# Optimization experiments

Hardware: AMD Instinct MI355X
Metric: run time of the kernel (lower is better)

The kernel has to match this reference:

```python
import jax, jax.numpy as jnp
import numpy as np

L, H, D, M = 2, 8, 64, 64   # layers, heads, query dim, value dim
DM = H * M                  # d_model = 512
FF = 1024                   # feed-forward dim
B, S, F_IN = 8, 4096, 586   # batch, seq_len, input feature dim
EPS_ATTN = 1e-6             # fast_transformers LinearAttention eps
EPS_LN = 1e-5               # torch LayerNorm default eps


def setup_inputs() -> dict:
    key = jax.random.key(0)
    ks = jax.random.split(key, 16)
    p = lambda k, shape: jax.random.normal(k, shape, jnp.float32) * 0.02
    return {
        "embeddings": jax.random.normal(ks[0], (B, S, F_IN), jnp.float32),
        "W0": p(ks[1], (F_IN, DM)), "b0": jnp.zeros((DM,), jnp.float32),
        "Wq": p(ks[2], (L, DM, DM)), "bq": jnp.zeros((L, DM), jnp.float32),
        "Wk": p(ks[3], (L, DM, DM)), "bk": jnp.zeros((L, DM), jnp.float32),
        "Wv": p(ks[4], (L, DM, DM)), "bv": jnp.zeros((L, DM), jnp.float32),
        "Wo": p(ks[5], (L, DM, DM)), "bo": jnp.zeros((L, DM), jnp.float32),
        "ln1_s": jnp.ones((L, DM), jnp.float32), "ln1_b": jnp.zeros((L, DM), jnp.float32),
        "W1": p(ks[6], (L, DM, FF)), "b1": jnp.zeros((L, FF), jnp.float32),
        "W2": p(ks[7], (L, FF, DM)), "b2": jnp.zeros((L, DM), jnp.float32),
        "ln2_s": jnp.ones((L, DM), jnp.float32), "ln2_b": jnp.zeros((L, DM), jnp.float32),
        "lnf_s": jnp.ones((DM,), jnp.float32), "lnf_b": jnp.zeros((DM,), jnp.float32),
        "Wout": p(ks[8], (DM, 1)), "bout": jnp.zeros((1,), jnp.float32),
    }


def _ln(x, s, b):
    mu = x.mean(-1, keepdims=True)
    var = ((x - mu) ** 2).mean(-1, keepdims=True)
    return (x - mu) * jax.lax.rsqrt(var + EPS_LN) * s + b


def _feat(x):
    # elu feature map of fast_transformers linear attention
    return jax.nn.elu(x) + 1.0


def reference(embeddings, W0, b0, Wq, bq, Wk, bk, Wv, bv, Wo, bo,
              ln1_s, ln1_b, W1, b1, W2, b2, ln2_s, ln2_b,
              lnf_s, lnf_b, Wout, bout):
    x = embeddings @ W0 + b0                       # [B,S,DM]
    Bn, Sn = x.shape[0], x.shape[1]
    for l in range(L):
        q = _feat((x @ Wq[l] + bq[l]).reshape(Bn, Sn, H, D))
        k = _feat((x @ Wk[l] + bk[l]).reshape(Bn, Sn, H, D))
        v = (x @ Wv[l] + bv[l]).reshape(Bn, Sn, H, M)
        # non-causal linear attention: O(S) in sequence length
        kv = jnp.einsum("bshd,bshm->bhdm", k, v)                    # [B,H,D,M]
        z = 1.0 / (jnp.einsum("blhd,bhd->blh", q, k.sum(1)) + EPS_ATTN)
        a = jnp.einsum("blhd,bhdm,blh->blhm", q, kv, z).reshape(Bn, Sn, DM)
        x = x + a @ Wo[l] + bo[l]                  # residual (dropout=0 eval)
        x = _ln(x, ln1_s[l], ln1_b[l])
        y = jax.nn.relu(x @ W1[l] + b1[l]) @ W2[l] + b2[l]
        x = _ln(x + y, ln2_s[l], ln2_b[l])
    x = _ln(x, lnf_s, lnf_b)                        # final encoder LayerNorm
    return (x @ Wout + bout)[..., 0]                # squeeze -> [B,S]
```

## Files before the change

### kernel.cpp

```cpp
#include <hip/hip_runtime.h>
#include <hip/hip_bf16.h>
#include <math.h>

typedef unsigned short u16;
typedef short s16x8 __attribute__((ext_vector_type(8)));
typedef float f32x4 __attribute__((ext_vector_type(4)));

#define BS_   32768
#define SEQ_  4096
#define DM_   512
#define FF_   1024
#define FIN_  586
#define FINP_ 608
#define PADC  136
#define PADB  520
#define NCH   8

__device__ __forceinline__ u16 f2b(float f) {
    __hip_bfloat16 h = __float2bfloat16(f);
    return *reinterpret_cast<u16*>(&h);
}
__device__ __forceinline__ float b2f(u16 h) {
    union { unsigned u; float f; } a; a.u = ((unsigned)h) << 16;
    return a.f;
}

typedef __attribute__((address_space(1))) const unsigned gu32;
typedef __attribute__((address_space(3))) unsigned lu32;
__device__ __forceinline__ void glds16(const void* g, void* l) {
    __builtin_amdgcn_global_load_lds((gu32*)g, (lu32*)l, 16, 0, 0);
}

__device__ __forceinline__ void tr_tile(const float* __restrict__ W, u16* __restrict__ Wt,
                                        int K, int N, int Kpad, int tidx, int ktiles,
                                        float (*t)[33]) {
    int kb = (tidx % ktiles) << 5, nb = (tidx / ktiles) << 5;
    int tx = threadIdx.x, ty = threadIdx.y;
#pragma unroll
    for (int j = 0; j < 32; j += 8) {
        int k = kb + ty + j;
        t[ty + j][tx] = (k < K) ? W[(size_t)k * N + nb + tx] : 0.f;
    }
    __syncthreads();
#pragma unroll
    for (int j = 0; j < 32; j += 8) {
        Wt[(size_t)(nb + ty + j) * Kpad + kb + tx] = f2b(t[tx][ty + j]);
    }
}

__global__ void k_tr_all(const float* __restrict__ W0, const float* __restrict__ Wq,
                         const float* __restrict__ Wk, const float* __restrict__ Wv,
                         const float* __restrict__ Wo, const float* __restrict__ W1,
                         const float* __restrict__ W2,
                         u16* __restrict__ W0t, u16* __restrict__ Wqkv,
                         u16* __restrict__ Wot, u16* __restrict__ W1t,
                         u16* __restrict__ W2t) {
    __shared__ float t[32][33];
    int b = blockIdx.x;
    if (b < 304) { tr_tile(W0, W0t, FIN_, DM_, FINP_, b, 19, t); return; }
    b -= 304;
    int l = b >> 11;
    int r = b & 2047;
    if (r < 768) {
        int sel = r >> 8, ti = r & 255;
        const float* src = sel == 0 ? Wq : (sel == 1 ? Wk : Wv);
        tr_tile(src + (size_t)l * 262144, Wqkv + (size_t)l * 786432 + (size_t)sel * 262144,
                512, 512, 512, ti, 16, t);
    } else if (r < 1024) {
        tr_tile(Wo + (size_t)l * 262144, Wot + (size_t)l * 262144, 512, 512, 512, r - 768, 16, t);
    } else if (r < 1536) {
        tr_tile(W1 + (size_t)l * 524288, W1t + (size_t)l * 524288, 512, 1024, 512, r - 1024, 16, t);
    } else {
        tr_tile(W2 + (size_t)l * 524288, W2t + (size_t)l * 524288, 1024, 512, 1024, r - 1536, 32, t);
    }
}

__global__ __launch_bounds__(256)
void k_emb(const float* __restrict__ E, u16* __restrict__ Ep) {
    const int total8 = BS_ * (FINP_ / 8);
    for (int i = blockIdx.x * 256 + threadIdx.x; i < total8; i += gridDim.x * 256) {
        int rr = i / (FINP_ / 8), c = (i % (FINP_ / 8)) * 8;
        const float* rp = E + (size_t)rr * FIN_ + c;
        s16x8 o;
#pragma unroll
        for (int e = 0; e < 8; ++e) {
            float v = (c + e < FIN_) ? rp[e] : 0.f;
            o[e] = (short)f2b(v);
        }
        *(s16x8*)(Ep + (size_t)rr * FINP_ + c) = o;
    }
}

template<int EPI>
__global__ __launch_bounds__(256, 4)
void k_gemm(const u16* __restrict__ A, const u16* __restrict__ Bt,
            const float* __restrict__ bias0, const float* __restrict__ bias1,
            const float* __restrict__ bias2,
            u16* __restrict__ out0, u16* __restrict__ out1, u16* __restrict__ out2,
            int M, int N, int K, int NT) {
    __shared__ __align__(16) u16 smem[16384];
    u16* sC = smem;

    const int nwg = gridDim.x;
    const int cpx = nwg >> 3;
    const int wg = (blockIdx.x & 7) * cpx + (blockIdx.x >> 3);
    const int mt = wg / NT, nt = wg - mt * NT;
    const int m0 = mt << 7, n0 = nt << 7;
    const int tid = threadIdx.x;
    const int w = tid >> 6, l = tid & 63;
    const int wm = (w >> 1) << 6, wn = (w & 1) << 6;
    const int lr = l & 15, lg = l >> 4;

    const int srow = tid >> 2;
    const int swz = (((tid & 3) ^ ((srow >> 1) & 3)) & 3) << 3;
    const u16* Ap = A + (size_t)(m0 + srow) * K + swz;
    const u16* Bp = Bt + (size_t)(n0 + srow) * K + swz;

    auto stage = [&](int d, int tt) {
        const size_t ko = (size_t)tt << 5;
        u16* da = smem + d * 4096 + tid * 8;
        u16* db = smem + 8192 + d * 4096 + tid * 8;
        glds16(Ap + ko, da);
        glds16(Ap + ko + (size_t)64 * K, da + 2048);
        glds16(Bp + ko, db);
        glds16(Bp + ko + (size_t)64 * K, db + 2048);
    };

    const int axk = ((lg ^ ((lr >> 1) & 3)) & 3) << 3;

    f32x4 acc[4][4] = {};
    const int ntile = K >> 5;

    stage(0, 0);
    __syncthreads();

    for (int t = 0; t < ntile; ++t) {
        const int d = t & 1;
        if (t + 1 < ntile) stage(d ^ 1, t + 1);
        const u16* sA = smem + d * 4096;
        const u16* sB = smem + 8192 + d * 4096;
        s16x8 af[4], bfr[4];
#pragma unroll
        for (int i = 0; i < 4; ++i) af[i] = *(const s16x8*)(sA + (wm + i * 16 + lr) * 32 + axk);
#pragma unroll
        for (int j = 0; j < 4; ++j) bfr[j] = *(const s16x8*)(sB + (wn + j * 16 + lr) * 32 + axk);
        __builtin_amdgcn_s_setprio(1);
#pragma unroll
        for (int i = 0; i < 4; ++i)
#pragma unroll
            for (int j = 0; j < 4; ++j)
                acc[i][j] = __builtin_amdgcn_mfma_f32_16x16x32_bf16(af[i], bfr[j], acc[i][j], 0, 0, 0);
        __builtin_amdgcn_s_setprio(0);
        __syncthreads();
    }

    const int seg = (EPI == 1) ? (n0 >> 9) : 0;
    const float* bias = (EPI == 1) ? (seg == 0 ? bias0 : (seg == 1 ? bias1 : bias2)) : bias0;
    u16* dst = (EPI == 1) ? (seg == 0 ? out0 : (seg == 1 ? out1 : out2)) : out0;
    const int ldo = (EPI == 1) ? 512 : N;
    const int ncol0 = (EPI == 1) ? (n0 & 511) : n0;

#pragma unroll
    for (int pass = 0; pass < 2; ++pass) {
        if ((w >> 1) == pass) {
#pragma unroll
            for (int j = 0; j < 4; ++j) {
                const int col = wn + j * 16 + lr;
                const float bv = bias[ncol0 + col];
#pragma unroll
                for (int i = 0; i < 4; ++i)
#pragma unroll
                    for (int r = 0; r < 4; ++r) {
                        const int row = i * 16 + (lg << 2) + r;
                        sC[row * PADC + col] = f2b(acc[i][j][r] + bv);
                    }
            }
        }
        __syncthreads();
        const int rbase = m0 + (pass << 6);
#pragma unroll
        for (int t = 0; t < 4; ++t) {
            const int idx = t * 256 + tid;
            const int row = idx >> 4;
            const int c8 = (idx & 15) << 3;
            s16x8 v8 = *(const s16x8*)(sC + row * PADC + c8);
            size_t gaddr = (size_t)(rbase + row) * ldo + ncol0 + c8;
            s16x8 o = v8;
            if constexpr (EPI == 1) {
                if (seg < 2) {
#pragma unroll
                    for (int e = 0; e < 8; ++e) {
                        float v = b2f((u16)v8[e]);
                        v = (v > 0.f) ? v + 1.f : __expf(v);
                        o[e] = (short)f2b(v);
                    }
                }
            } else if constexpr (EPI == 3) {
#pragma unroll
                for (int e = 0; e < 8; ++e)
                    o[e] = (short)f2b(fmaxf(b2f((u16)v8[e]), 0.f));
            }
            *(s16x8*)(dst + gaddr) = o;
        }
        __syncthreads();
    }
}

template<int K>
__global__ __launch_bounds__(512, 4)
void k_gemm_ln(const u16* __restrict__ A, const u16* __restrict__ Bt,
               const float* __restrict__ bias, const u16* __restrict__ resid,
               const float* __restrict__ g, const float* __restrict__ be,
               u16* __restrict__ xb) {
    __shared__ __align__(16) u16 smem[36864];
    u16* sC = smem;

    const int nwg = gridDim.x;
    const int cpx = nwg >> 3;
    const int wg = (blockIdx.x & 7) * cpx + (blockIdx.x >> 3);
    const int m0 = wg << 6;
    const int tid = threadIdx.x;
    const int w = tid >> 6, l = tid & 63;
    const int wn = w << 6;
    const int lr = l & 15, lg = l >> 4;

    const int srow = tid >> 2;
    const int swz = (((tid & 3) ^ ((srow >> 1) & 3)) & 3) << 3;
    const u16* ApA = A + (size_t)(m0 + (srow & 63)) * K + ((((tid & 3) ^ (((srow & 63) >> 1) & 3)) & 3) << 3);
    const u16* BpB = Bt + (size_t)srow * K + swz;

    auto stage = [&](int d, int tt) {
        const size_t ko = (size_t)tt << 5;
        if (tid < 256) glds16(ApA + ko, smem + d * 2048 + tid * 8);
#pragma unroll
        for (int c = 0; c < 4; ++c)
            glds16(BpB + ko + (size_t)(c * 128) * K,
                   smem + 4096 + d * 16384 + c * 4096 + tid * 8);
    };

    const int axk = ((lg ^ ((lr >> 1) & 3)) & 3) << 3;

    f32x4 acc[4][4] = {};
    const int ntile = K >> 5;

    stage(0, 0);
    __syncthreads();

    for (int t = 0; t < ntile; ++t) {
        const int d = t & 1;
        if (t + 1 < ntile) stage(d ^ 1, t + 1);
        const u16* sA = smem + d * 2048;
        const u16* sB = smem + 4096 + d * 16384 + wn * 32;
        s16x8 af[4], bfr[4];
#pragma unroll
        for (int i = 0; i < 4; ++i) af[i] = *(const s16x8*)(sA + (i * 16 + lr) * 32 + axk);
#pragma unroll
        for (int j = 0; j < 4; ++j) bfr[j] = *(const s16x8*)(sB + (j * 16 + lr) * 32 + axk);
        __builtin_amdgcn_s_setprio(1);
#pragma unroll
        for (int i = 0; i < 4; ++i)
#pragma unroll
            for (int j = 0; j < 4; ++j)
                acc[i][j] = __builtin_amdgcn_mfma_f32_16x16x32_bf16(af[i], bfr[j], acc[i][j], 0, 0, 0);
        __builtin_amdgcn_s_setprio(0);
        __syncthreads();
    }

#pragma unroll
    for (int j = 0; j < 4; ++j) {
        const int col = wn + j * 16 + lr;
        const float bv = bias[col];
#pragma unroll
        for (int i = 0; i < 4; ++i)
#pragma unroll
            for (int r = 0; r < 4; ++r) {
                const int row = i * 16 + (lg << 2) + r;
                sC[row * PADB + col] = f2b(acc[i][j][r] + bv);
            }
    }
    __syncthreads();

#pragma unroll
    for (int it = 0; it < 8; ++it) {
        const int row = it * 8 + w;
        s16x8 cv = *(const s16x8*)(sC + row * PADB + l * 8);
        s16x8 rv = *(const s16x8*)(resid + (size_t)(m0 + row) * DM_ + l * 8);
        float x[8];
#pragma unroll
        for (int e = 0; e < 8; ++e) x[e] = b2f((u16)cv[e]) + b2f((u16)rv[e]);
        float sum = 0.f;
#pragma unroll
        for (int e = 0; e < 8; ++e) sum += x[e];
#pragma unroll
        for (int off = 32; off > 0; off >>= 1) sum += __shfl_xor(sum, off);
        float mu = sum * (1.f / DM_);
        float sq = 0.f;
#pragma unroll
        for (int e = 0; e < 8; ++e) { float d = x[e] - mu; sq += d * d; }
#pragma unroll
        for (int off = 32; off > 0; off >>= 1) sq += __shfl_xor(sq, off);
        float rs = rsqrtf(sq * (1.f / DM_) + 1e-5f);
        const int c = l * 8;
        const f32x4* gp = (const f32x4*)(g + c);
        const f32x4* bp = (const f32x4*)(be + c);
        f32x4 g0 = gp[0], g1 = gp[1], e0 = bp[0], e1 = bp[1];
        s16x8 pk;
#pragma unroll
        for (int e = 0; e < 4; ++e) pk[e] = (short)f2b((x[e] - mu) * rs * g0[e] + e0[e]);
#pragma unroll
        for (int e = 0; e < 4; ++e) pk[4 + e] = (short)f2b((x[4 + e] - mu) * rs * g1[e] + e1[e]);
        *(s16x8*)(xb + (size_t)(m0 + row) * DM_ + c) = pk;
    }
}

__global__ __launch_bounds__(256)
void k_kv(const u16* __restrict__ kb_, const u16* __restrict__ vb_,
          float* __restrict__ kvp, float* __restrict__ ksump) {
    __shared__ float sk[64 * 68], sv[64 * 68];
    int bh = blockIdx.x, b = bh >> 3, h = bh & 7;
    int ch = blockIdx.y;
    int tid = threadIdx.x;
    int d0 = (tid & 15) << 2, m0 = (tid >> 4) << 2;
    float acc[4][4] = {};
    float ks[4] = {0.f, 0.f, 0.f, 0.f};
    size_t gbase = ((size_t)b * SEQ_ + (size_t)ch * (SEQ_ / NCH)) * DM_ + h * 64;

    for (int st = 0; st < SEQ_ / NCH; st += 64) {
#pragma unroll
        for (int i = 0; i < 2; ++i) {
            int li = tid + (i << 8);
            int r = li >> 3, c8 = (li & 7) << 3;
            s16x8 kv_ = *(const s16x8*)(kb_ + gbase + (size_t)(st + r) * DM_ + c8);
            s16x8 vv_ = *(const s16x8*)(vb_ + gbase + (size_t)(st + r) * DM_ + c8);
#pragma unroll
            for (int e = 0; e < 8; ++e) {
                sk[r * 68 + c8 + e] = b2f((u16)kv_[e]);
                sv[r * 68 + c8 + e] = b2f((u16)vv_[e]);
            }
        }
        __syncthreads();
        for (int s = 0; s < 64; ++s) {
            f32x4 kd = *(const f32x4*)(sk + s * 68 + d0);
            f32x4 vm = *(const f32x4*)(sv + s * 68 + m0);
#pragma unroll
            for (int i = 0; i < 4; ++i)
#pragma unroll
                for (int j = 0; j < 4; ++j) acc[i][j] += kd[i] * vm[j];
            if ((tid >> 4) == 0) { ks[0] += kd[0]; ks[1] += kd[1]; ks[2] += kd[2]; ks[3] += kd[3]; }
        }
        __syncthreads();
    }
    float* kvo = kvp + ((size_t)ch * 64 + bh) * 4096;
#pragma unroll
    for (int i = 0; i < 4; ++i)
#pragma unroll
        for (int j = 0; j < 4; ++j) kvo[(d0 + i) * 64 + m0 + j] = acc[i][j];
    if ((tid >> 4) == 0) {
        float* kso = ksump + ((size_t)ch * 64 + bh) * 64;
#pragma unroll
        for (int e = 0; e < 4; ++e) kso[d0 + e] = ks[e];
    }
}

__global__ __launch_bounds__(256)
void k_red(const float* __restrict__ kvp, const float* __restrict__ ksump,
           u16* __restrict__ kvt, float* __restrict__ ksum) {
    int bh = blockIdx.x, q = blockIdx.y;
    int tid = threadIdx.x;
#pragma unroll
    for (int p = 0; p < 4; ++p) {
        int i = (q * 4 + p) * 256 + tid;
        float v = 0.f;
#pragma unroll
        for (int c = 0; c < NCH; ++c) v += kvp[((size_t)c * 64 + bh) * 4096 + i];
        int d = i >> 6, m = i & 63;
        int slot = ((d >> 3) ^ (m & 7)) & 7;
        kvt[(size_t)bh * 4096 + m * 64 + slot * 8 + (d & 7)] = f2b(v);
    }
    if (q == 0 && tid < 64) {
        float v = 0.f;
#pragma unroll
        for (int c = 0; c < NCH; ++c) v += ksump[((size_t)c * 64 + bh) * 64 + tid];
        ksum[bh * 64 + tid] = v;
    }
}

__global__ __launch_bounds__(256)
void k_attn(const u16* __restrict__ qb_, const u16* __restrict__ kvt,
            const float* __restrict__ ksum, u16* __restrict__ ab_) {
    __shared__ __align__(16) u16 qs[256 * 64];
    __shared__ __align__(16) u16 skv[64 * 64];
    __shared__ float sden[256];
    __shared__ float sks[64];
    const int tid = threadIdx.x;
    const int bh = blockIdx.y, b = bh >> 3, h = bh & 7;
    const int s0 = blockIdx.x << 8;
    const int w = tid >> 6, l = tid & 63;
    const int lr = l & 15, lg = l >> 4;

    {
        const int srw = tid >> 3, ch = tid & 7;
        const int scol = ((ch ^ (srw & 7)) & 7) << 3;
        const u16* qsrc = qb_ + ((size_t)b * SEQ_ + s0 + srw) * DM_ + h * 64 + scol;
#pragma unroll
        for (int p = 0; p < 8; ++p)
            glds16(qsrc + (size_t)(p * 32) * DM_, qs + p * 2048 + tid * 8);
#pragma unroll
        for (int p = 0; p < 2; ++p)
            glds16(kvt + (size_t)bh * 4096 + p * 2048 + tid * 8, skv + p * 2048 + tid * 8);
    }
    if (tid < 64) sks[tid] = ksum[bh * 64 + tid];
    __syncthreads();

    {
        const int row = (w << 6) + l;
        float den = 0.f;
#pragma unroll
        for (int c = 0; c < 8; ++c) {
            s16x8 qv = *(const s16x8*)(qs + row * 64 + (((c ^ (row & 7)) & 7) << 3));
#pragma unroll
            for (int e = 0; e < 8; ++e) den += b2f((u16)qv[e]) * sks[c * 8 + e];
        }
        sden[row] = 1.f / (den + 1e-6f);
    }
    __syncthreads();

    f32x4 acc[4][4] = {};
#pragma unroll
    for (int kh = 0; kh < 2; ++kh) {
        const int c = kh * 4 + lg;
        s16x8 bfr[4];
#pragma unroll
        for (int j = 0; j < 4; ++j) {
            const int mm = j * 16 + lr;
            bfr[j] = *(const s16x8*)(skv + mm * 64 + (((c ^ (mm & 7)) & 7) << 3));
        }
#pragma unroll
        for (int i = 0; i < 4; ++i) {
            const int rr = (w << 6) + i * 16 + lr;
            s16x8 af = *(const s16x8*)(qs + rr * 64 + (((c ^ (rr & 7)) & 7) << 3));
#pragma unroll
            for (int j = 0; j < 4; ++j)
                acc[i][j] = __builtin_amdgcn_mfma_f32_16x16x32_bf16(af, bfr[j], acc[i][j], 0, 0, 0);
        }
    }
    __syncthreads();

#pragma unroll
    for (int i = 0; i < 4; ++i) {
#pragma unroll
        for (int r = 0; r < 4; ++r) {
            const int row = (w << 6) + i * 16 + (lg << 2) + r;
            const float z = sden[row];
#pragma unroll
            for (int j = 0; j < 4; ++j)
                qs[row * 64 + j * 16 + lr] = f2b(acc[i][j][r] * z);
        }
    }
    __syncthreads();
    {
        const int srw = tid >> 3, ch = tid & 7;
        u16* odst = ab_ + ((size_t)b * SEQ_ + s0 + srw) * DM_ + h * 64 + ch * 8;
#pragma unroll
        for (int p = 0; p < 8; ++p)
            *(s16x8*)(odst + (size_t)(p * 32) * DM_) = *(const s16x8*)(qs + p * 2048 + tid * 8);
    }
}

__global__ __launch_bounds__(256)
void k_final(const u16* __restrict__ in, const float* __restrict__ gf,
             const float* __restrict__ bf_, const float* __restrict__ wout,
             const float* __restrict__ bout, float* __restrict__ out) {
    int row = blockIdx.x * 4 + (threadIdx.x >> 6);
    int l = threadIdx.x & 63;
    s16x8 raw = *(const s16x8*)(in + (size_t)row * DM_ + l * 8);
    float x[8];
#pragma unroll
    for (int e = 0; e < 8; ++e) x[e] = b2f((u16)raw[e]);
    float sum = 0.f;
#pragma unroll
    for (int e = 0; e < 8; ++e) sum += x[e];
#pragma unroll
    for (int off = 32; off > 0; off >>= 1) sum += __shfl_xor(sum, off);
    float mu = sum * (1.f / DM_);
    float sq = 0.f;
#pragma unroll
    for (int e = 0; e < 8; ++e) { float d = x[e] - mu; sq += d * d; }
#pragma unroll
    for (int off = 32; off > 0; off >>= 1) sq += __shfl_xor(sq, off);
    float rs = rsqrtf(sq * (1.f / DM_) + 1e-5f);
    int c = l * 8;
    float p = 0.f;
#pragma unroll
    for (int e = 0; e < 8; ++e)
        p += ((x[e] - mu) * rs * gf[c + e] + bf_[c + e]) * wout[c + e];
#pragma unroll
    for (int off = 32; off > 0; off >>= 1) p += __shfl_xor(p, off);
    if (l == 0) out[row] = p + bout[0];
}

extern "C" void kernel_launch(void* const* d_in, const int* in_sizes, int n_in,
                              void* d_out, int out_size, void* d_ws, size_t ws_size,
                              hipStream_t stream) {
    const float* emb   = (const float*)d_in[0];
    const float* W0    = (const float*)d_in[1];
    const float* b0    = (const float*)d_in[2];
    const float* Wq    = (const float*)d_in[3];
    const float* bq    = (const float*)d_in[4];
    const float* Wk    = (const float*)d_in[5];
    const float* bk    = (const float*)d_in[6];
    const float* Wv    = (const float*)d_in[7];
    const float* bv    = (const float*)d_in[8];
    const float* Wo    = (const float*)d_in[9];
    const float* bo    = (const float*)d_in[10];
    const float* ln1s  = (const float*)d_in[11];
    const float* ln1b  = (const float*)d_in[12];
    const float* W1    = (const float*)d_in[13];
    const float* b1    = (const float*)d_in[14];
    const float* W2    = (const float*)d_in[15];
    const float* b2    = (const float*)d_in[16];
    const float* ln2s  = (const float*)d_in[17];
    const float* ln2b  = (const float*)d_in[18];
    const float* lnfs  = (const float*)d_in[19];
    const float* lnfb  = (const float*)d_in[20];
    const float* Wout  = (const float*)d_in[21];
    const float* bout  = (const float*)d_in[22];
    float* out = (float*)d_out;

    char* ws = (char*)d_ws;
    size_t off = 0;
    auto alloc = [&](size_t bytes) -> void* {
        void* p = ws + off;
        off += (bytes + 255) & ~(size_t)255;
        return p;
    };
    u16* xb   = (u16*)alloc((size_t)BS_ * DM_ * 2);
    u16* qb   = (u16*)alloc((size_t)BS_ * DM_ * 2);
    u16* kb   = (u16*)alloc((size_t)BS_ * DM_ * 2);
    u16* vb   = (u16*)alloc((size_t)BS_ * DM_ * 2);
    float* kvp   = (float*)alloc((size_t)NCH * 64 * 4096 * 4);
    float* ksump = (float*)alloc((size_t)NCH * 64 * 64 * 4);
    u16* kvt  = (u16*)alloc((size_t)64 * 4096 * 2);
    float* ksum = (float*)alloc((size_t)64 * 64 * 4);
    u16* wp   = (u16*)alloc((size_t)4521984 * 2);

    u16* ab   = vb;
    u16* h1b  = kb;
    u16* embp = kb;

    u16* W0t  = wp;
    u16* Wqkv = wp + 311296;
    u16* Wot  = Wqkv + 2 * 786432;
    u16* W1t  = Wot + 2 * 262144;
    u16* W2t  = W1t + 2 * 524288;

    k_tr_all<<<4400, dim3(32, 8), 0, stream>>>(W0, Wq, Wk, Wv, Wo, W1, W2,
                                               W0t, Wqkv, Wot, W1t, W2t);
    k_emb<<<2560, 256, 0, stream>>>(emb, embp);

    k_gemm<0><<<1024, 256, 0, stream>>>(embp, W0t, b0, nullptr, nullptr,
                                        xb, nullptr, nullptr, BS_, DM_, FINP_, 4);

    for (int l = 0; l < 2; ++l) {
        k_gemm<1><<<3072, 256, 0, stream>>>(xb, Wqkv + (size_t)l * 786432,
                                            bq + l * 512, bk + l * 512, bv + l * 512,
                                            qb, kb, vb, BS_, 1536, 512, 12);
        k_kv<<<dim3(64, NCH), 256, 0, stream>>>(kb, vb, kvp, ksump);
        k_red<<<dim3(64, 4), 256, 0, stream>>>(kvp, ksump, kvt, ksum);
        k_attn<<<dim3(16, 64), 256, 0, stream>>>(qb, kvt, ksum, ab);
        k_gemm_ln<512><<<512, 512, 0, stream>>>(ab, Wot + (size_t)l * 262144,
                                                bo + l * 512, xb,
                                                ln1s + l * 512, ln1b + l * 512, xb);
        k_gemm<3><<<2048, 256, 0, stream>>>(xb, W1t + (size_t)l * 524288,
                                            b1 + l * 1024, nullptr, nullptr,
                                            h1b, nullptr, nullptr, BS_, 1024, 512, 8);
        k_gemm_ln<1024><<<512, 512, 0, stream>>>(h1b, W2t + (size_t)l * 524288,
                                                 b2 + l * 512, xb,
                                                 ln2s + l * 512, ln2b + l * 512, xb);
    }
    k_final<<<8192, 256, 0, stream>>>(xb, lnfs, lnfb, Wout, bout, out);
}
```

Before: 591.8 us.

## Stage GEMM tiles per wave to drop workgroup barriers in the K loop

Each wave now loads its own A and B sub-tiles into a private shared-memory region and waits only on its own loads, removing the per-iteration __syncthreads. The shared double buffer and software prefetch are gone, so global loads no longer overlap with MFMA work inside a wave. Waves that share rows or columns now fetch the same data separately, which doubles global/L2 traffic per workgroup.

```diff
diff --git a/kernel.cpp b/kernel.cpp
--- a/kernel.cpp
+++ b/kernel.cpp
@@ -111,39 +111,32 @@
     const int wm = (w >> 1) << 6, wn = (w & 1) << 6;
     const int lr = l & 15, lg = l >> 4;
 
-    const int srow = tid >> 2;
-    const int swz = (((tid & 3) ^ ((srow >> 1) & 3)) & 3) << 3;
-    const u16* Ap = A + (size_t)(m0 + srow) * K + swz;
-    const u16* Bp = Bt + (size_t)(n0 + srow) * K + swz;
-
-    auto stage = [&](int d, int tt) {
-        const size_t ko = (size_t)tt << 5;
-        u16* da = smem + d * 4096 + tid * 8;
-        u16* db = smem + 8192 + d * 4096 + tid * 8;
-        glds16(Ap + ko, da);
-        glds16(Ap + ko + (size_t)64 * K, da + 2048);
-        glds16(Bp + ko, db);
-        glds16(Bp + ko + (size_t)64 * K, db + 2048);
-    };
+    u16* wA = smem + w * 4096;
+    u16* wB = wA + 2048;
+
+    const int srcswz = (((l & 3) ^ ((l >> 3) & 3)) & 3) << 3;
+    const u16* Awp = A + (size_t)(m0 + wm + (l >> 2)) * K + srcswz;
+    const u16* Bwp = Bt + (size_t)(n0 + wn + (l >> 2)) * K + srcswz;
 
     const int axk = ((lg ^ ((lr >> 1) & 3)) & 3) << 3;
 
     f32x4 acc[4][4] = {};
     const int ntile = K >> 5;
 
-    stage(0, 0);
-    __syncthreads();
-
     for (int t = 0; t < ntile; ++t) {
-        const int d = t & 1;
-        if (t + 1 < ntile) stage(d ^ 1, t + 1);
-        const u16* sA = smem + d * 4096;
-        const u16* sB = smem + 8192 + d * 4096;
+        const size_t ko = (size_t)t << 5;
+#pragma unroll
+        for (int g = 0; g < 4; ++g) {
+            glds16(Awp + ko + (size_t)(g * 16) * K, wA + g * 512 + l * 8);
+            glds16(Bwp + ko + (size_t)(g * 16) * K, wB + g * 512 + l * 8);
+        }
+        asm volatile("s_waitcnt vmcnt(0)" ::: "memory");
+        __builtin_amdgcn_sched_barrier(0);
         s16x8 af[4], bfr[4];
 #pragma unroll
-        for (int i = 0; i < 4; ++i) af[i] = *(const s16x8*)(sA + (wm + i * 16 + lr) * 32 + axk);
-#pragma unroll
-        for (int j = 0; j < 4; ++j) bfr[j] = *(const s16x8*)(sB + (wn + j * 16 + lr) * 32 + axk);
+        for (int i = 0; i < 4; ++i) af[i] = *(const s16x8*)(wA + (i * 16 + lr) * 32 + axk);
+#pragma unroll
+        for (int j = 0; j < 4; ++j) bfr[j] = *(const s16x8*)(wB + (j * 16 + lr) * 32 + axk);
         __builtin_amdgcn_s_setprio(1);
 #pragma unroll
         for (int i = 0; i < 4; ++i)
@@ -151,8 +144,9 @@
             for (int j = 0; j < 4; ++j)
                 acc[i][j] = __builtin_amdgcn_mfma_f32_16x16x32_bf16(af[i], bfr[j], acc[i][j], 0, 0, 0);
         __builtin_amdgcn_s_setprio(0);
-        __syncthreads();
-    }
+        __builtin_amdgcn_sched_barrier(0);
+    }
+    __syncthreads();
 
     const int seg = (EPI == 1) ? (n0 >> 9) : 0;
     const float* bias = (EPI == 1) ? (seg == 0 ? bias0 : (seg == 1 ? bias1 : bias2)) : bias0;
```

Result: slower. 678.2 us (median of 3 runs) (+14.6%).
